# Kernel optimization log

Hardware: AMD Instinct MI355X
Metric: run time of the kernel (lower is better)

## Reference

```python
import jax, jax.numpy as jnp
import numpy as np

DEMBED = 512
DMODEL = 512
HEAD = 8
B, L = 4, 2048


def setup_inputs() -> dict:
    key = jax.random.key(0)
    ks = jax.random.split(key, 12)
    s_in = 1.0 / np.sqrt(DEMBED)
    s_out = 1.0 / np.sqrt(DMODEL)
    return {
        "x_q": jax.random.normal(ks[0], (B, L, DEMBED), jnp.float32),
        "x_k": jax.random.normal(ks[1], (B, L, DEMBED), jnp.float32),
        "x_v": jax.random.normal(ks[2], (B, L, DEMBED), jnp.float32),
        "mask": jax.random.randint(ks[3], (B, L, L), 0, 2, jnp.int32),
        "Wq": jax.random.uniform(ks[4], (DMODEL, DEMBED), jnp.float32, -s_in, s_in),
        "bq": jnp.zeros((DMODEL,), jnp.float32),
        "Wk": jax.random.uniform(ks[5], (DMODEL, DEMBED), jnp.float32, -s_in, s_in),
        "bk": jnp.zeros((DMODEL,), jnp.float32),
        "Wv": jax.random.uniform(ks[6], (DMODEL, DEMBED), jnp.float32, -s_in, s_in),
        "bv": jnp.zeros((DMODEL,), jnp.float32),
        "Wo": jax.random.uniform(ks[7], (DEMBED, DMODEL), jnp.float32, -s_out, s_out),
        "bo": jnp.zeros((DEMBED,), jnp.float32),
    }


def _split_heads(x):
    # [B, L, D] -> [B, head, L, h_dv]; head h gets contiguous channels h*h_dv:(h+1)*h_dv,
    # matching torch's transpose(1,2).reshape(B,head,h_dv,L).transpose(2,3)
    b, l, d = x.shape
    return x.reshape(b, l, HEAD, d // HEAD).transpose(0, 2, 1, 3)


def reference(x_q, x_k, x_v, mask, Wq, bq, Wk, bk, Wv, bv, Wo, bo):
    q = _split_heads(x_q @ Wq.T + bq)  # [B, H, L, hd]
    k = _split_heads(x_k @ Wk.T + bk)
    v = _split_heads(x_v @ Wv.T + bv)
    h_dv = q.shape[-1]
    scores = jnp.einsum("bhqd,bhkd->bhqk", q, k) / np.sqrt(h_dv)
    scores = scores + mask[:, None, :, :].astype(scores.dtype) * (-1e30)
    attn = jax.nn.softmax(scores, axis=-1)
    out = jnp.einsum("bhqk,bhkd->bhqd", attn, v)  # [B, H, L, hd]
    out = out.transpose(0, 2, 1, 3).reshape(x_q.shape[0], x_q.shape[1], DMODEL)
    final = out @ Wo.T + bo
    return final, attn
```

## Files before the change

kernel.cpp:

```cpp
#include <hip/hip_runtime.h>

typedef unsigned short u16;
typedef __attribute__((ext_vector_type(8))) short short8;
typedef __attribute__((ext_vector_type(4))) float f32x4;

#define DE 512
#define SL 2048
#define NB 4
#define NH 8
#define HD 64

__device__ __forceinline__ float bf2f(u16 h) {
    union { unsigned u; float f; } v; v.u = ((unsigned)h) << 16; return v.f;
}
__device__ __forceinline__ u16 f2bf(float f) {
    union { float f; unsigned u; } v; v.f = f;
    unsigned u = v.u;
    return (u16)((u + 0x7FFFu + ((u >> 16) & 1u)) >> 16);
}
__device__ __forceinline__ short8 ld8f(const float* __restrict__ p) {
    const float4 a = *(const float4*)p;
    const float4 b = *(const float4*)(p + 4);
    short8 r;
    ((u16*)&r)[0] = f2bf(a.x); ((u16*)&r)[1] = f2bf(a.y);
    ((u16*)&r)[2] = f2bf(a.z); ((u16*)&r)[3] = f2bf(a.w);
    ((u16*)&r)[4] = f2bf(b.x); ((u16*)&r)[5] = f2bf(b.y);
    ((u16*)&r)[6] = f2bf(b.z); ((u16*)&r)[7] = f2bf(b.w);
    return r;
}

__global__ __launch_bounds__(256) void cvt3(const float* __restrict__ s0,
                                            const float* __restrict__ s1,
                                            const float* __restrict__ s2,
                                            u16* __restrict__ dst, int per) {
    const float* src = (blockIdx.y == 0) ? s0 : ((blockIdx.y == 1) ? s1 : s2);
    const int idx = (blockIdx.x * 256 + threadIdx.x) * 8;
    if (idx >= per) return;
    short8 v = ld8f(src + idx);
    *(short8*)(dst + (size_t)blockIdx.y * per + idx) = v;
}

__device__ __forceinline__ void llds16(const u16* g, u16* l) {
    __builtin_amdgcn_global_load_lds((const __attribute__((address_space(1))) void*)g,
                                     (__attribute__((address_space(3))) void*)l, 16, 0, 0);
}

__device__ __forceinline__ void gemm64_body(u16* As, u16* Bs,
                                            const u16* __restrict__ X,
                                            const u16* __restrict__ W,
                                            const float* __restrict__ bias,
                                            void* __restrict__ outv,
                                            int mode, int tok0, int col0) {
    const int tid = threadIdx.x;
    const int l = tid & 63, w = tid >> 6;
    const int q16 = l & 15, quad = l >> 4;
    const int wr = w >> 1, wc = w & 1;

    const int srow = tid >> 3;
    const int scol = ((tid & 7) ^ (srow & 7)) * 8;
    const u16* ga = X + (size_t)(tok0 + srow) * DE + scol;
    const u16* gb = W + (size_t)(col0 + srow) * DE + scol;
    u16* la = As + tid * 8;
    u16* lb = Bs + tid * 8;

    f32x4 acc[2][2] = {};

    #pragma unroll
    for (int i = 0; i < 2; ++i) {
        llds16(ga + (size_t)i * 32 * DE, la + i * 2048);
        llds16(gb + (size_t)i * 32 * DE, lb + i * 2048);
    }
    __syncthreads();

    int cur = 0;
    for (int ks = 64; ks <= DE; ks += 64) {
        if (ks < DE) {
            u16* da = la + (cur ^ 1) * 4096;
            u16* db = lb + (cur ^ 1) * 4096;
            #pragma unroll
            for (int i = 0; i < 2; ++i) {
                llds16(ga + (size_t)i * 32 * DE + ks, da + i * 2048);
                llds16(gb + (size_t)i * 32 * DE + ks, db + i * 2048);
            }
        }
        const char* Ab = (const char*)(As + cur * 4096);
        const char* Bb = (const char*)(Bs + cur * 4096);
        #pragma unroll
        for (int kk = 0; kk < 64; kk += 32) {
            short8 af[2], bf[2];
            #pragma unroll
            for (int m = 0; m < 2; ++m) {
                const int row = wr * 32 + m * 16 + q16;
                af[m] = *(const short8*)(Ab + row * 128 + (((kk + quad * 8) * 2) ^ ((q16 & 7) << 4)));
            }
            #pragma unroll
            for (int n = 0; n < 2; ++n) {
                const int row = wc * 32 + n * 16 + q16;
                bf[n] = *(const short8*)(Bb + row * 128 + (((kk + quad * 8) * 2) ^ ((q16 & 7) << 4)));
            }
            #pragma unroll
            for (int m = 0; m < 2; ++m)
                #pragma unroll
                for (int n = 0; n < 2; ++n)
                    acc[m][n] = __builtin_amdgcn_mfma_f32_16x16x32_bf16(af[m], bf[n], acc[m][n], 0, 0, 0);
        }
        __syncthreads();
        cur ^= 1;
    }

    #pragma unroll
    for (int n = 0; n < 2; ++n) {
        const int col = col0 + wc * 32 + n * 16 + q16;
        const float bv = bias[col];
        #pragma unroll
        for (int m = 0; m < 2; ++m) {
            const f32x4 a4 = acc[m][n];
            const int tg0 = tok0 + wr * 32 + m * 16 + quad * 4;
            if (mode == 2) {
                const int b = tg0 >> 11, t0 = tg0 & 2047;
                const int h = col >> 6, d = col & 63;
                ushort4 pk;
                pk.x = f2bf(a4[0] + bv); pk.y = f2bf(a4[1] + bv);
                pk.z = f2bf(a4[2] + bv); pk.w = f2bf(a4[3] + bv);
                *(ushort4*)((u16*)outv + ((size_t)((b * NH + h) * HD + d) << 11) + t0) = pk;
            } else if (mode == 1) {
                const int h = col >> 6, d = col & 63;
                #pragma unroll
                for (int r = 0; r < 4; ++r) {
                    const int tg = tg0 + r;
                    const int b = tg >> 11, t = tg & 2047;
                    ((u16*)outv)[(((size_t)(b * NH + h) * SL + t) << 6) + d] = f2bf(a4[r] + bv);
                }
            } else {
                #pragma unroll
                for (int r = 0; r < 4; ++r)
                    ((float*)outv)[(size_t)(tg0 + r) * DE + col] = a4[r] + bv;
            }
        }
    }
}

__global__ __launch_bounds__(256) void gemm_qkv(const u16* __restrict__ xbf,
                                                const u16* __restrict__ wbf,
                                                const float* __restrict__ bq,
                                                const float* __restrict__ bk,
                                                const float* __restrict__ bv,
                                                u16* __restrict__ outbase) {
    __shared__ __align__(16) u16 As[2][4096];
    __shared__ __align__(16) u16 Bs[2][4096];
    const int z = blockIdx.z;
    const u16* X = xbf + (size_t)z * 4194304;
    const u16* W = wbf + (size_t)z * 262144;
    const float* bias = (z == 0) ? bq : ((z == 1) ? bk : bv);
    u16* out = outbase + (size_t)z * 4194304;
    gemm64_body(&As[0][0], &Bs[0][0], X, W, bias, out,
                (z == 2) ? 2 : 1, blockIdx.x * 64, blockIdx.y * 64);
}

__global__ __launch_bounds__(256) void gemm_fin(const u16* __restrict__ X,
                                                const u16* __restrict__ W,
                                                const float* __restrict__ bias,
                                                float* __restrict__ outp) {
    __shared__ __align__(16) u16 As[2][4096];
    __shared__ __align__(16) u16 Bs[2][4096];
    gemm64_body(&As[0][0], &Bs[0][0], X, W, bias, outp,
                0, blockIdx.x * 64, blockIdx.y * 64);
}

__global__ __launch_bounds__(512) void attn_kernel(const u16* __restrict__ Q,
                                                   const u16* __restrict__ K,
                                                   const u16* __restrict__ Vt,
                                                   const int* __restrict__ mask,
                                                   float* __restrict__ attn_out,
                                                   u16* __restrict__ Obuf) {
    __shared__ __align__(16) u16 P[16][2056];
    __shared__ float partial[16][8];
    __shared__ float linv[16];
    __shared__ float ored[4][16][16];

    const int tid = threadIdx.x;
    const int lane = tid & 63, wave = tid >> 6;
    const int q16 = lane & 15, quad = lane >> 4;

    const int p = blockIdx.x;
    const int x8 = p & 7, n = p >> 3;
    const int h = n & 7;
    const int r = x8 + ((n >> 3) << 3);
    const int qblk = r >> 2, b = r & 3;
    const int qbase = qblk * 16;

    const u16* qplane = Q + (size_t)((b * NH + h) * SL) * HD;
    const u16* kplane = K + (size_t)((b * NH + h) * SL) * HD;

    const u16* qrow = qplane + (qbase + q16) * HD + quad * 8;
    const short8 aq0 = *(const short8*)(qrow);
    const short8 aq1 = *(const short8*)(qrow + 32);

    const int k0 = wave * 256;
    const int* mrowp = mask + (size_t)(b * SL + qbase + q16) * SL;
    float rs = 0.f;

    #pragma unroll 4
    for (int kt = 0; kt < 16; ++kt) {
        const int kb = k0 + kt * 16;
        const u16* krow = kplane + (kb + q16) * HD + quad * 8;
        const short8 b0 = *(const short8*)(krow);
        const short8 b1 = *(const short8*)(krow + 32);
        const int4 m4 = *(const int4*)(mrowp + kb + quad * 4);

        f32x4 s = {};
        s = __builtin_amdgcn_mfma_f32_16x16x32_bf16(b0, aq0, s, 0, 0, 0);
        s = __builtin_amdgcn_mfma_f32_16x16x32_bf16(b1, aq1, s, 0, 0, 0);

        const float u0 = m4.x ? 0.0f : __expf(s[0] * 0.125f);
        const float u1 = m4.y ? 0.0f : __expf(s[1] * 0.125f);
        const float u2 = m4.z ? 0.0f : __expf(s[2] * 0.125f);
        const float u3 = m4.w ? 0.0f : __expf(s[3] * 0.125f);
        rs += (u0 + u1) + (u2 + u3);
        uint2 pk;
        pk.x = (unsigned)f2bf(u0) | ((unsigned)f2bf(u1) << 16);
        pk.y = (unsigned)f2bf(u2) | ((unsigned)f2bf(u3) << 16);
        *(uint2*)&P[q16][kb + quad * 4] = pk;
    }
    rs += __shfl_xor(rs, 16);
    rs += __shfl_xor(rs, 32);
    if (lane < 16) partial[lane][wave] = rs;
    __syncthreads();

    if (tid < 16) {
        float s = 0.f;
        #pragma unroll
        for (int w = 0; w < 8; ++w) s += partial[tid][w];
        linv[tid] = 1.0f / s;
    }
    __syncthreads();

    {
        const int r3 = tid >> 5, cseg = tid & 31;
        const float inv = linv[r3];
        const size_t rowbase = ((size_t)((b * NH + h) * SL + qbase + r3)) * SL;
        #pragma unroll
        for (int i = 0; i < 8; ++i) {
            const int c = cseg * 8 + i * 256;
            short8 v = *(const short8*)&P[r3][c];
            f32x4 w0, w1;
            w0[0] = bf2f(((u16*)&v)[0]) * inv;
            w0[1] = bf2f(((u16*)&v)[1]) * inv;
            w0[2] = bf2f(((u16*)&v)[2]) * inv;
            w0[3] = bf2f(((u16*)&v)[3]) * inv;
            w1[0] = bf2f(((u16*)&v)[4]) * inv;
            w1[1] = bf2f(((u16*)&v)[5]) * inv;
            w1[2] = bf2f(((u16*)&v)[6]) * inv;
            w1[3] = bf2f(((u16*)&v)[7]) * inv;
            __builtin_nontemporal_store(w0, (f32x4*)(attn_out + rowbase + c));
            __builtin_nontemporal_store(w1, (f32x4*)(attn_out + rowbase + c + 4));
        }
    }

    const int dt = wave & 3, kh = wave >> 2;
    const u16* vplane = Vt + (size_t)((b * NH + h) * HD) * SL;
    f32x4 o = {};
    const int kstart = kh * 1024;
    #pragma unroll 4
    for (int kk = kstart; kk < kstart + 1024; kk += 32) {
        short8 a = *(const short8*)&P[q16][kk + quad * 8];
        short8 bv = *(const short8*)(vplane + (dt * 16 + q16) * SL + kk + quad * 8);
        o = __builtin_amdgcn_mfma_f32_16x16x32_bf16(a, bv, o, 0, 0, 0);
    }
    if (kh == 1) {
        #pragma unroll
        for (int rr = 0; rr < 4; ++rr) ored[dt][quad * 4 + rr][q16] = o[rr];
    }
    __syncthreads();
    if (kh == 0) {
        #pragma unroll
        for (int rr = 0; rr < 4; ++rr) {
            const int row = quad * 4 + rr;
            const float val = (o[rr] + ored[dt][row][q16]) * linv[row];
            const int qg = qbase + row;
            Obuf[(size_t)(b * SL + qg) * DE + h * HD + dt * 16 + q16] = f2bf(val);
        }
    }
}

extern "C" void kernel_launch(void* const* d_in, const int* in_sizes, int n_in,
                              void* d_out, int out_size, void* d_ws, size_t ws_size,
                              hipStream_t stream) {
    const float* x_q = (const float*)d_in[0];
    const float* x_k = (const float*)d_in[1];
    const float* x_v = (const float*)d_in[2];
    const int* mask = (const int*)d_in[3];
    const float* Wq = (const float*)d_in[4];
    const float* bq = (const float*)d_in[5];
    const float* Wk = (const float*)d_in[6];
    const float* bk = (const float*)d_in[7];
    const float* Wv = (const float*)d_in[8];
    const float* bv = (const float*)d_in[9];
    const float* Wo = (const float*)d_in[10];
    const float* bo = (const float*)d_in[11];

    u16* ws = (u16*)d_ws;
    u16* qb = ws;
    u16* vt = ws + 2 * 4194304;
    u16* ob = ws + 3 * 4194304;

    float* outp = (float*)d_out;
    float* attn_out = outp + 4194304;

    u16* xbf = (u16*)attn_out;
    u16* wbf = xbf + 3 * 4194304;

    cvt3<<<dim3(2048, 3), 256, 0, stream>>>(x_q, x_k, x_v, xbf, 4194304);
    cvt3<<<dim3(128, 3), 256, 0, stream>>>(Wq, Wk, Wv, wbf, 262144);

    gemm_qkv<<<dim3(128, 8, 3), 256, 0, stream>>>(xbf, wbf, bq, bk, bv, ws);

    attn_kernel<<<dim3(4096), 512, 0, stream>>>(qb, ws + 4194304, vt, mask, attn_out, ob);

    cvt3<<<dim3(128, 1), 256, 0, stream>>>(Wo, Wo, Wo, qb, 262144);
    gemm_fin<<<dim3(128, 8), 256, 0, stream>>>(ob, qb, bo, outp);
}
```

Before: 933.4 us.

## Recompute scores in registers and fuse attn write with PV, dropping LDS P buffer

The attention kernel no longer stages unnormalized probabilities in a 64KB shared-memory P buffer. After computing row sums, each wave recomputes QK^T and exp for its key range, writes the normalized attention directly, and feeds the packed bf16 probabilities straight into PV MFMAs. To make the register layout match the MFMA operand, the V-transposed output of the QKV GEMM is written with a permuted token order. Per-wave partial outputs are then reduced through a smaller LDS buffer. This trades a second QK^T and exp pass, plus a second read of K and mask, for less LDS use and higher occupancy. The launch grid also changes from a swizzled 1D order to a plain 3D order, which alters block scheduling and cache locality.

New measurement: 1.050 ms. 1.13x slower.

```diff
diff --git a/kernel.cpp b/kernel.cpp
--- a/kernel.cpp
+++ b/kernel.cpp
@@ -118,11 +118,12 @@
             const int tg0 = tok0 + wr * 32 + m * 16 + quad * 4;
             if (mode == 2) {
                 const int b = tg0 >> 11, t0 = tg0 & 2047;
+                const int t0p = (t0 & ~31) | ((t0 & 12) << 1) | ((t0 & 16) >> 2);
                 const int h = col >> 6, d = col & 63;
                 ushort4 pk;
                 pk.x = f2bf(a4[0] + bv); pk.y = f2bf(a4[1] + bv);
                 pk.z = f2bf(a4[2] + bv); pk.w = f2bf(a4[3] + bv);
-                *(ushort4*)((u16*)outv + ((size_t)((b * NH + h) * HD + d) << 11) + t0) = pk;
+                *(ushort4*)((u16*)outv + ((size_t)((b * NH + h) * HD + d) << 11) + t0p) = pk;
             } else if (mode == 1) {
                 const int h = col >> 6, d = col & 63;
                 #pragma unroll
@@ -173,24 +174,19 @@
                                                    const int* __restrict__ mask,
                                                    float* __restrict__ attn_out,
                                                    u16* __restrict__ Obuf) {
-    __shared__ __align__(16) u16 P[16][2056];
     __shared__ float partial[16][8];
     __shared__ float linv[16];
-    __shared__ float ored[4][16][16];
+    __shared__ float Ored[8][16][65];
 
     const int tid = threadIdx.x;
     const int lane = tid & 63, wave = tid >> 6;
     const int q16 = lane & 15, quad = lane >> 4;
-
-    const int p = blockIdx.x;
-    const int x8 = p & 7, n = p >> 3;
-    const int h = n & 7;
-    const int r = x8 + ((n >> 3) << 3);
-    const int qblk = r >> 2, b = r & 3;
+    const int qblk = blockIdx.x, h = blockIdx.y, b = blockIdx.z;
     const int qbase = qblk * 16;
 
     const u16* qplane = Q + (size_t)((b * NH + h) * SL) * HD;
     const u16* kplane = K + (size_t)((b * NH + h) * SL) * HD;
+    const u16* vplane = Vt + (size_t)((b * NH + h) * HD) * SL;
 
     const u16* qrow = qplane + (qbase + q16) * HD + quad * 8;
     const short8 aq0 = *(const short8*)(qrow);
@@ -198,8 +194,8 @@
 
     const int k0 = wave * 256;
     const int* mrowp = mask + (size_t)(b * SL + qbase + q16) * SL;
+
     float rs = 0.f;
-
     #pragma unroll 4
     for (int kt = 0; kt < 16; ++kt) {
         const int kb = k0 + kt * 16;
@@ -207,26 +203,19 @@
         const short8 b0 = *(const short8*)(krow);
         const short8 b1 = *(const short8*)(krow + 32);
         const int4 m4 = *(const int4*)(mrowp + kb + quad * 4);
-
         f32x4 s = {};
         s = __builtin_amdgcn_mfma_f32_16x16x32_bf16(b0, aq0, s, 0, 0, 0);
         s = __builtin_amdgcn_mfma_f32_16x16x32_bf16(b1, aq1, s, 0, 0, 0);
-
         const float u0 = m4.x ? 0.0f : __expf(s[0] * 0.125f);
         const float u1 = m4.y ? 0.0f : __expf(s[1] * 0.125f);
         const float u2 = m4.z ? 0.0f : __expf(s[2] * 0.125f);
         const float u3 = m4.w ? 0.0f : __expf(s[3] * 0.125f);
         rs += (u0 + u1) + (u2 + u3);
-        uint2 pk;
-        pk.x = (unsigned)f2bf(u0) | ((unsigned)f2bf(u1) << 16);
-        pk.y = (unsigned)f2bf(u2) | ((unsigned)f2bf(u3) << 16);
-        *(uint2*)&P[q16][kb + quad * 4] = pk;
     }
     rs += __shfl_xor(rs, 16);
     rs += __shfl_xor(rs, 32);
     if (lane < 16) partial[lane][wave] = rs;
     __syncthreads();
-
     if (tid < 16) {
         float s = 0.f;
         #pragma unroll
@@ -234,52 +223,81 @@
         linv[tid] = 1.0f / s;
     }
     __syncthreads();
-
+    const float inv = linv[q16];
+
+    f32x4 o0 = {}, o1 = {}, o2 = {}, o3 = {};
+    const size_t arowbase = ((size_t)((b * NH + h) * SL + qbase + q16)) * SL;
+    #pragma unroll 2
+    for (int c = 0; c < 8; ++c) {
+        const int kb = k0 + c * 32;
+        const u16* kr0 = kplane + (kb + q16) * HD + quad * 8;
+        const short8 b0 = *(const short8*)(kr0);
+        const short8 b1 = *(const short8*)(kr0 + 32);
+        const int4 m4a = *(const int4*)(mrowp + kb + quad * 4);
+        f32x4 s = {};
+        s = __builtin_amdgcn_mfma_f32_16x16x32_bf16(b0, aq0, s, 0, 0, 0);
+        s = __builtin_amdgcn_mfma_f32_16x16x32_bf16(b1, aq1, s, 0, 0, 0);
+        const float u0 = m4a.x ? 0.0f : __expf(s[0] * 0.125f);
+        const float u1 = m4a.y ? 0.0f : __expf(s[1] * 0.125f);
+        const float u2 = m4a.z ? 0.0f : __expf(s[2] * 0.125f);
+        const float u3 = m4a.w ? 0.0f : __expf(s[3] * 0.125f);
+        f32x4 w0; w0[0] = u0 * inv; w0[1] = u1 * inv; w0[2] = u2 * inv; w0[3] = u3 * inv;
+        __builtin_nontemporal_store(w0, (f32x4*)(attn_out + arowbase + kb + quad * 4));
+        uint2 pk0;
+        pk0.x = (unsigned)f2bf(u0) | ((unsigned)f2bf(u1) << 16);
+        pk0.y = (unsigned)f2bf(u2) | ((unsigned)f2bf(u3) << 16);
+
+        const u16* kr1 = kplane + (kb + 16 + q16) * HD + quad * 8;
+        const short8 c0 = *(const short8*)(kr1);
+        const short8 c1 = *(const short8*)(kr1 + 32);
+        const int4 m4b = *(const int4*)(mrowp + kb + 16 + quad * 4);
+        f32x4 t = {};
+        t = __builtin_amdgcn_mfma_f32_16x16x32_bf16(c0, aq0, t, 0, 0, 0);
+        t = __builtin_amdgcn_mfma_f32_16x16x32_bf16(c1, aq1, t, 0, 0, 0);
+        const float v0 = m4b.x ? 0.0f : __expf(t[0] * 0.125f);
+        const float v1 = m4b.y ? 0.0f : __expf(t[1] * 0.125f);
+        const float v2 = m4b.z ? 0.0f : __expf(t[2] * 0.125f);
+        const float v3 = m4b.w ? 0.0f : __expf(t[3] * 0.125f);
+        f32x4 w1; w1[0] = v0 * inv; w1[1] = v1 * inv; w1[2] = v2 * inv; w1[3] = v3 * inv;
+        __builtin_nontemporal_store(w1, (f32x4*)(attn_out + arowbase + kb + 16 + quad * 4));
+        uint2 pk1;
+        pk1.x = (unsigned)f2bf(v0) | ((unsigned)f2bf(v1) << 16);
+        pk1.y = (unsigned)f2bf(v2) | ((unsigned)f2bf(v3) << 16);
+
+        union { uint4 u; short8 s8; } af;
+        af.u.x = pk0.x; af.u.y = pk0.y; af.u.z = pk1.x; af.u.w = pk1.y;
+        const u16* vb = vplane + (size_t)q16 * SL + kb + quad * 8;
+        const short8 bv0 = *(const short8*)(vb);
+        const short8 bv1 = *(const short8*)(vb + 16 * SL);
+        const short8 bv2 = *(const short8*)(vb + 32 * SL);
+        const short8 bv3 = *(const short8*)(vb + 48 * SL);
+        o0 = __builtin_amdgcn_mfma_f32_16x16x32_bf16(af.s8, bv0, o0, 0, 0, 0);
+        o1 = __builtin_amdgcn_mfma_f32_16x16x32_bf16(af.s8, bv1, o1, 0, 0, 0);
+        o2 = __builtin_amdgcn_mfma_f32_16x16x32_bf16(af.s8, bv2, o2, 0, 0, 0);
+        o3 = __builtin_amdgcn_mfma_f32_16x16x32_bf16(af.s8, bv3, o3, 0, 0, 0);
+    }
+
+    #pragma unroll
+    for (int r = 0; r < 4; ++r) {
+        Ored[wave][quad * 4 + r][q16]      = o0[r];
+        Ored[wave][quad * 4 + r][16 + q16] = o1[r];
+        Ored[wave][quad * 4 + r][32 + q16] = o2[r];
+        Ored[wave][quad * 4 + r][48 + q16] = o3[r];
+    }
+    __syncthreads();
     {
-        const int r3 = tid >> 5, cseg = tid & 31;
-        const float inv = linv[r3];
-        const size_t rowbase = ((size_t)((b * NH + h) * SL + qbase + r3)) * SL;
+        const int qq = tid >> 5, d0 = (tid & 31) * 2;
+        float a0 = 0.f, a1 = 0.f;
         #pragma unroll
-        for (int i = 0; i < 8; ++i) {
-            const int c = cseg * 8 + i * 256;
-            short8 v = *(const short8*)&P[r3][c];
-            f32x4 w0, w1;
-            w0[0] = bf2f(((u16*)&v)[0]) * inv;
-            w0[1] = bf2f(((u16*)&v)[1]) * inv;
-            w0[2] = bf2f(((u16*)&v)[2]) * inv;
-            w0[3] = bf2f(((u16*)&v)[3]) * inv;
-            w1[0] = bf2f(((u16*)&v)[4]) * inv;
-            w1[1] = bf2f(((u16*)&v)[5]) * inv;
-            w1[2] = bf2f(((u16*)&v)[6]) * inv;
-            w1[3] = bf2f(((u16*)&v)[7]) * inv;
-            __builtin_nontemporal_store(w0, (f32x4*)(attn_out + rowbase + c));
-            __builtin_nontemporal_store(w1, (f32x4*)(attn_out + rowbase + c + 4));
+        for (int w = 0; w < 8; ++w) {
+            a0 += Ored[w][qq][d0];
+            a1 += Ored[w][qq][d0 + 1];
         }
-    }
-
-    const int dt = wave & 3, kh = wave >> 2;
-    const u16* vplane = Vt + (size_t)((b * NH + h) * HD) * SL;
-    f32x4 o = {};
-    const int kstart = kh * 1024;
-    #pragma unroll 4
-    for (int kk = kstart; kk < kstart + 1024; kk += 32) {
-        short8 a = *(const short8*)&P[q16][kk + quad * 8];
-        short8 bv = *(const short8*)(vplane + (dt * 16 + q16) * SL + kk + quad * 8);
-        o = __builtin_amdgcn_mfma_f32_16x16x32_bf16(a, bv, o, 0, 0, 0);
-    }
-    if (kh == 1) {
-        #pragma unroll
-        for (int rr = 0; rr < 4; ++rr) ored[dt][quad * 4 + rr][q16] = o[rr];
-    }
-    __syncthreads();
-    if (kh == 0) {
-        #pragma unroll
-        for (int rr = 0; rr < 4; ++rr) {
-            const int row = quad * 4 + rr;
-            const float val = (o[rr] + ored[dt][row][q16]) * linv[row];
-            const int qg = qbase + row;
-            Obuf[(size_t)(b * SL + qg) * DE + h * HD + dt * 16 + q16] = f2bf(val);
-        }
+        const float iv = linv[qq];
+        ushort2 pk;
+        pk.x = f2bf(a0 * iv);
+        pk.y = f2bf(a1 * iv);
+        *(ushort2*)&Obuf[(size_t)(b * SL + qbase + qq) * DE + h * HD + d0] = pk;
     }
 }
 
@@ -315,7 +333,7 @@
 
     gemm_qkv<<<dim3(128, 8, 3), 256, 0, stream>>>(xbf, wbf, bq, bk, bv, ws);
 
-    attn_kernel<<<dim3(4096), 512, 0, stream>>>(qb, ws + 4194304, vt, mask, attn_out, ob);
+    attn_kernel<<<dim3(128, 8, 4), 512, 0, stream>>>(qb, ws + 4194304, vt, mask, attn_out, ob);
 
     cvt3<<<dim3(128, 1), 256, 0, stream>>>(Wo, Wo, Wo, qb, 262144);
     gemm_fin<<<dim3(128, 8), 256, 0, stream>>>(ob, qb, bo, outp);
```
